# Performance work log

Measured on AMD Instinct MI355X. Metric: run time of the kernel, lower is better.

The kernel has to match this reference:

```python
import jax, jax.numpy as jnp
import numpy as np

DIM = 512
DIM2 = 2 * DIM
HEADS = 8
HEAD_DIM = DIM2 // HEADS
NB = 4                      # BlockDiagonalLinear blocks
BLK = DIM2 // NB
KS = 4                      # causal conv kernel size
EPS = 1e-5


def setup_inputs() -> dict:
    key = jax.random.key(0)
    ks = jax.random.split(key, 32)
    r = lambda i, shape, s=0.02: jax.random.normal(ks[i], shape, dtype=jnp.float32) * s
    inp = {
        "x": jax.random.normal(ks[0], (2, 2048, DIM), dtype=jnp.float32),
        "ln_w": jnp.ones((DIM,), jnp.float32),
        "ln_b": jnp.zeros((DIM,), jnp.float32),
        "mlp1_w": r(1, (DIM, DIM2)), "mlp1_b": jnp.zeros((DIM2,), jnp.float32),
        "mlp2_w": r(2, (DIM, DIM2)), "mlp2_b": jnp.zeros((DIM2,), jnp.float32),
        "conv_w": r(3, (DIM2, DIM2, KS)), "conv_b": jnp.zeros((DIM2,), jnp.float32),
        "bq_w": r(4, (NB, BLK, BLK)), "bk_w": r(5, (NB, BLK, BLK)), "bv_w": r(6, (NB, BLK, BLK)),
        "wq_w": r(7, (DIM2, DIM2)), "wq_b": jnp.zeros((DIM2,), jnp.float32),
        "wk_w": r(8, (DIM2, DIM2)), "wk_b": jnp.zeros((DIM2,), jnp.float32),
        "wv_w": r(9, (DIM2, DIM2)), "wv_b": jnp.zeros((DIM2,), jnp.float32),
        "wi_w": r(10, (DIM2, HEADS)), "wi_b": jnp.zeros((HEADS,), jnp.float32),
        "wf_w": r(11, (DIM2, HEADS)), "wf_b": jnp.zeros((HEADS,), jnp.float32),
        "gn_w": jnp.ones((DIM2,), jnp.float32), "gn_b": jnp.zeros((DIM2,), jnp.float32),
        "skip": jnp.ones((DIM2,), jnp.float32),
        "fin_w": r(12, (DIM2, DIM)), "fin_b": jnp.zeros((DIM,), jnp.float32),
    }
    return inp


def _layernorm(x, w, b):
    mu = jnp.mean(x, -1, keepdims=True)
    var = jnp.var(x, -1, keepdims=True)
    return (x - mu) * jax.lax.rsqrt(var + EPS) * w + b


def _block_linear(x, w):  # x: [b,s,DIM2], w: [NB, BLK, BLK]
    b, s, _ = x.shape
    xg = x.reshape(b, s, NB, BLK)
    return jnp.einsum('bsgi,gio->bsgo', xg, w).reshape(b, s, DIM2)


def _mlstm_cell(q, k, v, wq_w, wq_b, wk_w, wk_b, wv_w, wv_b,
                wi_w, wi_b, wf_w, wf_b, gn_w, gn_b):
    b, s, _ = q.shape
    tau = DIM2 ** 0.5
    itilde = jnp.einsum('bsd,dh->bhs', q, wi_w) + wi_b[None, :, None]   # [b,h,s]
    ftilde = jnp.einsum('bsd,dh->bhs', k, wf_w) + wf_b[None, :, None]   # [b,h,s]
    # cumulative log forget gates; F_act[i,j] = cs[i] - cs[j] on lower triangle
    cs = jnp.cumsum(jax.nn.log_sigmoid(ftilde), axis=-1)                # [b,h,s]
    mask = jnp.tril(jnp.ones((s, s), bool))
    Dtilde = jnp.where(mask,
                       cs[..., :, None] - cs[..., None, :] + itilde[..., None, :],
                       -jnp.inf)                                        # [b,h,s,s]
    max_d = jnp.max(Dtilde, axis=-1, keepdims=True)
    D = jnp.exp(Dtilde - max_d)
    qh = (q @ wq_w + wq_b).reshape(b, s, HEADS, HEAD_DIM).transpose(0, 2, 1, 3)
    kh = (k @ wk_w + wk_b).reshape(b, s, HEADS, HEAD_DIM).transpose(0, 2, 1, 3)
    vh = (v @ wv_w + wv_b).reshape(b, s, HEADS, HEAD_DIM).transpose(0, 2, 1, 3)
    Ctilde = jnp.einsum('bhid,bhjd->bhij', qh, kh) * D / tau
    maxit = jnp.maximum(jnp.abs(Ctilde.sum(-1)), jnp.exp(-max_d[..., 0]))  # [b,h,s]
    H = jnp.einsum('bhij,bhjd->bhid', Ctilde, vh) / (maxit[..., None] + 1e-8)
    H = H.transpose(0, 2, 1, 3)                                          # [b,s,h,hd]
    # GroupNorm(heads, DIM2): per (b,s,head-group) normalization
    mu = jnp.mean(H, -1, keepdims=True)
    var = jnp.var(H, -1, keepdims=True)
    Hn = (H - mu) * jax.lax.rsqrt(var + EPS)
    Hn = Hn * gn_w.reshape(HEADS, HEAD_DIM) + gn_b.reshape(HEADS, HEAD_DIM)
    return Hn.reshape(b, s, DIM2)


def reference(x, ln_w, ln_b, mlp1_w, mlp1_b, mlp2_w, mlp2_b, conv_w, conv_b,
              bq_w, bk_w, bv_w, wq_w, wq_b, wk_w, wk_b, wv_w, wv_b,
              wi_w, wi_b, wf_w, wf_b, gn_w, gn_b, skip, fin_w, fin_b):
    inputs = _layernorm(x, ln_w, ln_b)
    a = inputs @ mlp1_w + mlp1_b                 # [b,s,DIM2]
    bgate = jax.nn.silu(inputs @ mlp2_w + mlp2_b)
    # causal conv1d (left pad KS-1)
    ac = a.transpose(0, 2, 1)                    # [b,DIM2,s]
    qk = jax.lax.conv_general_dilated(ac, conv_w, (1,), [(KS - 1, 0)],
                                      dimension_numbers=('NCH', 'OIH', 'NCH'))
    qk = (qk + conv_b[None, :, None]).transpose(0, 2, 1)
    qk = jax.nn.silu(qk)
    q = _block_linear(qk, bq_w)
    k = _block_linear(qk, bk_w)
    v = _block_linear(a, bv_w)
    out1 = _mlstm_cell(q, k, v, wq_w, wq_b, wk_w, wk_b, wv_w, wv_b,
                       wi_w, wi_b, wf_w, wf_b, gn_w, gn_b)
    out1 = out1 + skip * qk
    out1 = out1 * bgate
    out1 = out1 @ fin_w + fin_b
    return x + out1
```

## Files before the change

### kernel.cpp

```cpp
#include <hip/hip_runtime.h>
#include <hip/hip_bf16.h>
#include <cmath>

typedef __hip_bfloat16 bf16;
typedef __attribute__((ext_vector_type(8))) short short8;
typedef __attribute__((ext_vector_type(4))) float f32x4;

#define SEQ   2048
#define DIMX  512
#define DIM2X 1024
#define NHEADS 8
#define HDIM  128
#define EPSF  1e-5f
#define PADROWS 2051

__device__ __forceinline__ float b2f(bf16 v) { return __bfloat162float(v); }
__device__ __forceinline__ bf16 f2b(float f) { return __float2bfloat16(f); }
__device__ __forceinline__ unsigned short f2bu(float f) { bf16 t = __float2bfloat16(f); return *(unsigned short*)&t; }

__device__ __forceinline__ void gl16(const bf16* g, bf16* l) {
  __builtin_amdgcn_global_load_lds((const __attribute__((address_space(1))) void*)g,
                                   (__attribute__((address_space(3))) void*)l, 16, 0, 0);
}

__global__ void __launch_bounds__(256) k_layernorm(const float* __restrict__ x,
                                                   const float* __restrict__ w,
                                                   const float* __restrict__ b,
                                                   bf16* __restrict__ out) {
  int row  = blockIdx.x * 4 + (threadIdx.x >> 6);
  int lane = threadIdx.x & 63;
  const float* xr = x + (size_t)row * DIMX;
  float v[8]; float s = 0.f, sq = 0.f;
#pragma unroll
  for (int i = 0; i < 8; i++) {
    float f = xr[lane + i * 64];
    v[i] = f; s += f; sq += f * f;
  }
#pragma unroll
  for (int off = 32; off; off >>= 1) { s += __shfl_xor(s, off); sq += __shfl_xor(sq, off); }
  float mu  = s * (1.f / DIMX);
  float var = sq * (1.f / DIMX) - mu * mu;
  float rs  = rsqrtf(var + EPSF);
  bf16* o = out + (size_t)row * DIMX;
#pragma unroll
  for (int i = 0; i < 8; i++) {
    int c = lane + i * 64;
    o[c] = f2b((v[i] - mu) * rs * w[c] + b[c]);
  }
}

__global__ void __launch_bounds__(256) k_castT3(const float* __restrict__ W0,
                                                const float* __restrict__ W1,
                                                const float* __restrict__ W2,
                                                bf16* __restrict__ WT,
                                                int K, int N, int innerZ, int gW, int gT) {
  __shared__ float t[32][33];
  const int z = blockIdx.z;
  const int sel = z / innerZ, zz = z % innerZ;
  const float* W = (sel == 0 ? W0 : sel == 1 ? W1 : W2) + (size_t)zz * gW;
  bf16* T = WT + (size_t)(sel * innerZ + zz) * gT;
  const int k0 = blockIdx.y * 32, n0 = blockIdx.x * 32;
  const int r = threadIdx.x >> 5, c = threadIdx.x & 31;
#pragma unroll
  for (int i = 0; i < 4; i++)
    t[r + i * 8][c] = W[(size_t)(k0 + r + i * 8) * N + n0 + c];
  __syncthreads();
#pragma unroll
  for (int i = 0; i < 4; i++)
    T[(size_t)(n0 + r + i * 8) * K + k0 + c] = f2b(t[c][r + i * 8]);
}

__global__ void __launch_bounds__(256) k_convwT(const float* __restrict__ cw, bf16* __restrict__ wc) {
  int idx = blockIdx.x * 256 + threadIdx.x;
  int o = idx >> 12, z = idx & 4095, kk = z >> 10, i = z & 1023;
  wc[idx] = f2b(cw[(size_t)o * 4096 + i * 4 + kk]);
}

__global__ void __launch_bounds__(256) k_zeropad(bf16* __restrict__ p) {
  int idx = blockIdx.x * 256 + threadIdx.x;
  int b = idx / 3072, off = idx % 3072;
  p[(size_t)b * PADROWS * DIM2X + off] = f2b(0.f);
}

__device__ __forceinline__ void mgemm_body(const bf16* A, int lda, const bf16* WT,
                                           const float* bias, void* Cv, const float* xres,
                                           int ldc, int K, int ACT, int STORE, int APAD,
                                           size_t coff) {
  __shared__ __align__(16) bf16 smA[128 * 32];
  __shared__ __align__(16) bf16 smB[64 * 32];
  const int tid  = threadIdx.x;
  const int lane = tid & 63;
  const int w = tid >> 6, wy = w >> 1, wx = w & 1;
  const int col = lane & 15, quad = lane >> 4;
  const int bm = blockIdx.y * 128, bn = blockIdx.x * 64;

  const int r4 = tid >> 2, c8 = (tid & 3) * 8;
  int ra0 = bm + r4, ra1 = bm + 64 + r4;
  if (APAD) { ra0 += (ra0 >> 11) * 3 + 3; ra1 += (ra1 >> 11) * 3 + 3; }
  const bf16* gA0 = A + (size_t)ra0 * lda + c8;
  const bf16* gA1 = A + (size_t)ra1 * lda + c8;
  const bf16* gB0 = WT + (size_t)(bn + r4) * K + c8;
  bf16* lA = &smA[r4 * 32 + c8];
  bf16* lB = &smB[r4 * 32 + c8];

  f32x4 acc[4][2];
#pragma unroll
  for (int a = 0; a < 4; a++)
#pragma unroll
    for (int b = 0; b < 2; b++) acc[a][b] = (f32x4){0.f, 0.f, 0.f, 0.f};

  const int laoff = (wy * 64) * 32, lboff = (wx * 32) * 32;
  for (int k0 = 0; k0 < K; k0 += 32) {
    gl16(gA0 + k0, lA);
    gl16(gA1 + k0, lA + 64 * 32);
    gl16(gB0 + k0, lB);
    asm volatile("s_waitcnt vmcnt(0)" ::: "memory");
    __syncthreads();
    short8 af[4], bfr[2];
#pragma unroll
    for (int mt = 0; mt < 4; mt++)
      af[mt] = *(const short8*)&smA[laoff + (mt * 16 + col) * 32 + quad * 8];
#pragma unroll
    for (int nt = 0; nt < 2; nt++)
      bfr[nt] = *(const short8*)&smB[lboff + (nt * 16 + col) * 32 + quad * 8];
#pragma unroll
    for (int mt = 0; mt < 4; mt++)
#pragma unroll
      for (int nt = 0; nt < 2; nt++)
        acc[mt][nt] = __builtin_amdgcn_mfma_f32_16x16x32_bf16(af[mt], bfr[nt], acc[mt][nt], 0, 0, 0);
    __syncthreads();
  }

#pragma unroll
  for (int mt = 0; mt < 4; mt++) {
#pragma unroll
    for (int nt = 0; nt < 2; nt++) {
      const int n = bn + wx * 32 + nt * 16 + col;
      const int mrow0 = bm + wy * 64 + mt * 16 + quad * 4;
      float bs = bias ? bias[n] : 0.f;
      if (STORE == 1) {
        bf16* C = (bf16*)Cv + coff;
        ushort4 pk;
        pk.x = f2bu(acc[mt][nt][0] + bs); pk.y = f2bu(acc[mt][nt][1] + bs);
        pk.z = f2bu(acc[mt][nt][2] + bs); pk.w = f2bu(acc[mt][nt][3] + bs);
        *(ushort4*)(C + (size_t)n * 4096 + mrow0) = pk;
      } else if (STORE == 2) {
        float* O = (float*)Cv + coff;
#pragma unroll
        for (int r = 0; r < 4; r++) {
          size_t gi = (size_t)(mrow0 + r) * ldc + n;
          O[gi] = acc[mt][nt][r] + bs + xres[gi];
        }
      } else if (STORE == 3) {
        bf16* C = (bf16*)Cv;
        const int pr = (mrow0 >> 11) * 3 + 3;
#pragma unroll
        for (int r = 0; r < 4; r++)
          C[(size_t)(mrow0 + pr + r) * ldc + n] = f2b(acc[mt][nt][r] + bs);
      } else {
        bf16* C = (bf16*)Cv + coff;
#pragma unroll
        for (int r = 0; r < 4; r++) {
          float v = acc[mt][nt][r] + bs;
          if (ACT == 1) v = v / (1.f + expf(-v));
          C[(size_t)(mrow0 + r) * ldc + n] = f2b(v);
        }
      }
    }
  }
}

template <int ACT, int STORE, int APAD>
__global__ void __launch_bounds__(256) k_mgemm(const bf16* __restrict__ A, int lda,
                                               const bf16* __restrict__ WT,
                                               const float* __restrict__ bias,
                                               void* __restrict__ Cv,
                                               const float* __restrict__ xres,
                                               int ldc, int K,
                                               int gA, int gW, int gC) {
  const int g = blockIdx.z;
  mgemm_body(A + (size_t)g * gA, lda, WT + (size_t)g * gW, bias, Cv, xres,
             ldc, K, ACT, STORE, APAD, (size_t)g * gC);
}

__global__ void __launch_bounds__(256) k_mgemmB(const bf16* A0, const bf16* A1, const bf16* A2,
                                                const bf16* W0, const bf16* W1, const bf16* W2,
                                                const float* b0, const float* b1, const float* b2,
                                                void* C0, void* C1, void* C2,
                                                int lda, int ldc, int K, int zPer,
                                                int gA, int gW, int gC,
                                                int actm, int storem, int apadm) {
  const int z = blockIdx.z;
  const int sel = z / zPer, zz = z % zPer;
  const bf16* A = (sel == 0 ? A0 : sel == 1 ? A1 : A2) + (size_t)zz * gA;
  const bf16* W = (sel == 0 ? W0 : sel == 1 ? W1 : W2) + (size_t)zz * gW;
  const float* bias = sel == 0 ? b0 : sel == 1 ? b1 : b2;
  void* Cv = sel == 0 ? C0 : sel == 1 ? C1 : C2;
  mgemm_body(A, lda, W, bias, Cv, nullptr, ldc, K,
             (actm >> sel) & 1, (storem >> (4 * sel)) & 15, (apadm >> sel) & 1,
             (size_t)zz * gC);
}

__global__ void __launch_bounds__(256) k_gates(const bf16* __restrict__ q, const bf16* __restrict__ kk,
                                               const float* __restrict__ wi, const float* __restrict__ wib,
                                               const float* __restrict__ wf, const float* __restrict__ wfb,
                                               float* __restrict__ it, float* __restrict__ ft) {
  int gid  = blockIdx.x * 4 + (threadIdx.x >> 6);
  int lane = threadIdx.x & 63;
  int which = gid >> 12;
  int m = gid & 4095;
  const bf16* row = (which ? kk : q) + (size_t)m * DIM2X;
  const float* w = which ? wf : wi;
  float s[8] = {0, 0, 0, 0, 0, 0, 0, 0};
  for (int d = lane; d < DIM2X; d += 64) {
    float xv = b2f(row[d]);
    const float4* wp = (const float4*)(w + d * 8);
    float4 w0 = wp[0], w1 = wp[1];
    s[0] += xv * w0.x; s[1] += xv * w0.y; s[2] += xv * w0.z; s[3] += xv * w0.w;
    s[4] += xv * w1.x; s[5] += xv * w1.y; s[6] += xv * w1.z; s[7] += xv * w1.w;
  }
#pragma unroll
  for (int off = 32; off; off >>= 1) {
#pragma unroll
    for (int h = 0; h < 8; h++) s[h] += __shfl_xor(s[h], off);
  }
  if (lane == 0) {
    int b_ = m >> 11, tt = m & 2047;
    const float* wb = which ? wfb : wib;
    float* dst = which ? ft : it;
#pragma unroll
    for (int h = 0; h < 8; h++)
      dst[((size_t)(b_ * NHEADS + h)) * SEQ + tt] = s[h] + wb[h];
  }
}

__global__ void __launch_bounds__(256) k_scan(const float* __restrict__ it, const float* __restrict__ ft,
                                              float* __restrict__ cs, float* __restrict__ md) {
  const int bh = blockIdx.x;
  const int t  = threadIdx.x;
  const float* fr = ft + (size_t)bh * SEQ;
  const float* ir = it + (size_t)bh * SEQ;
  float* csr = cs + (size_t)bh * SEQ;
  float* mdr = md + (size_t)bh * SEQ;
  __shared__ float tmp[256];
  float loc[8]; float run = 0.f;
#pragma unroll
  for (int j = 0; j < 8; j++) {
    float xv = fr[t * 8 + j];
    float ls = fminf(xv, 0.f) - log1pf(expf(-fabsf(xv)));
    run += ls; loc[j] = run;
  }
  tmp[t] = run;
  __syncthreads();
  for (int off = 1; off < 256; off <<= 1) {
    float add = (t >= off) ? tmp[t - off] : 0.f;
    __syncthreads();
    tmp[t] += add;
    __syncthreads();
  }
  float exc = (t == 0) ? 0.f : tmp[t - 1];
  float csv[8];
#pragma unroll
  for (int j = 0; j < 8; j++) { csv[j] = loc[j] + exc; csr[t * 8 + j] = csv[j]; }
  __syncthreads();
  float rmax = -INFINITY; float gm[8];
#pragma unroll
  for (int j = 0; j < 8; j++) {
    float gv = ir[t * 8 + j] - csv[j];
    rmax = fmaxf(rmax, gv); gm[j] = rmax;
  }
  tmp[t] = rmax;
  __syncthreads();
  for (int off = 1; off < 256; off <<= 1) {
    float other = (t >= off) ? tmp[t - off] : -INFINITY;
    __syncthreads();
    tmp[t] = fmaxf(tmp[t], other);
    __syncthreads();
  }
  float emax = (t == 0) ? -INFINITY : tmp[t - 1];
#pragma unroll
  for (int j = 0; j < 8; j++) mdr[t * 8 + j] = csv[j] + fmaxf(gm[j], emax);
}

__global__ void __launch_bounds__(256) k_attn_mfma(const bf16* __restrict__ qh,
                                                   const bf16* __restrict__ kh,
                                                   const bf16* __restrict__ vt,
                                                   const float* __restrict__ cs,
                                                   const float* __restrict__ md,
                                                   const float* __restrict__ itl,
                                                   bf16* __restrict__ Hout) {
  const int bh = blockIdx.y, b_ = bh >> 3, h = bh & 7;
  const int tile = 31 - blockIdx.x;
  const int i0 = tile * 64;
  const int tid = threadIdx.x;
  const int w = tid >> 6;
  const int lane = tid & 63;
  const int col = lane & 15, quad = lane >> 4;
  const int i0w = i0 + w * 16;
  const int iwmax = i0w + 15;
  const float L2E = 1.44269504f;

  __shared__ __align__(16) bf16 smK[2 * 4096];
  __shared__ __align__(16) bf16 smV[2 * 4096];
  __shared__ __align__(16) bf16 Sc[4][16][40];

  const size_t baseQK = ((size_t)b_ * SEQ) * DIM2X + (size_t)h * HDIM;
  const size_t vtb = (size_t)(h * HDIM) * 4096 + (size_t)b_ * SEQ;
  const float* csp = cs + (size_t)bh * SEQ;
  const float* mdp = md + (size_t)bh * SEQ;
  const float* itp = itl + (size_t)bh * SEQ;

  short8 qf[4];
#pragma unroll
  for (int kc = 0; kc < 4; kc++)
    qf[kc] = *(const short8*)(qh + baseQK + (size_t)(i0w + col) * DIM2X + kc * 32 + quad * 8);

  float cs_i[4], md_i[4];
#pragma unroll
  for (int r = 0; r < 4; r++) {
    int i = i0w + quad * 4 + r;
    cs_i[r] = csp[i] * L2E; md_i[r] = mdp[i] * L2E;
  }

  f32x4 accpv[8];
#pragma unroll
  for (int nb = 0; nb < 8; nb++) accpv[nb] = (f32x4){0.f, 0.f, 0.f, 0.f};
  float rs[4] = {0.f, 0.f, 0.f, 0.f};

  const int kj = tid >> 4, kq = tid & 15;
  const bf16* gKs = kh + baseQK + (size_t)kj * DIM2X + ((kq ^ (kj & 7)) * 8);
  const int vn = tid >> 2, vq = tid & 3;
  const bf16* gVs = vt + vtb + (size_t)vn * 4096 + ((vq ^ ((vn >> 1) & 3)) * 8);

  const int trips = 2 * tile + 2;

#define STAGE(buf, j0s)                                                        \
  do {                                                                         \
    bf16* dK = &smK[(buf) * 4096 + tid * 8];                                   \
    gl16(gKs + (size_t)(j0s) * DIM2X, dK);                                     \
    gl16(gKs + (size_t)((j0s) + 16) * DIM2X, dK + 2048);                       \
    bf16* dV = &smV[(buf) * 4096 + tid * 8];                                   \
    gl16(gVs + (j0s), dV);                                                     \
    gl16(gVs + (j0s) + (size_t)64 * 4096, dV + 2048);                          \
  } while (0)

  STAGE(0, 0);
  asm volatile("s_waitcnt vmcnt(0)" ::: "memory");
  __syncthreads();

  for (int t = 0; t < trips; ++t) {
    const int cur = t & 1;
    const int j0p = t * 32;
    if (t + 1 < trips) STAGE(cur ^ 1, j0p + 32);
    if (j0p <= iwmax) {
      float g0 = (itp[j0p + col] - csp[j0p + col]) * L2E;
      float g1 = (itp[j0p + 16 + col] - csp[j0p + 16 + col]) * L2E;
      const bool jt1 = (j0p + 16 <= iwmax);
#pragma unroll
      for (int jt = 0; jt < 2; jt++) {
        const int j0 = j0p + jt * 16;
        float sv[4] = {0.f, 0.f, 0.f, 0.f};
        if (jt == 0 || jt1) {
          const int jj = jt * 16 + col;
          f32x4 aq = (f32x4){0.f, 0.f, 0.f, 0.f};
#pragma unroll
          for (int kc = 0; kc < 4; kc++) {
            short8 bk = *(const short8*)&smK[cur * 4096 + jj * 128 + ((((kc << 2) | quad) ^ (jj & 7)) << 3)];
            aq = __builtin_amdgcn_mfma_f32_16x16x32_bf16(qf[kc], bk, aq, 0, 0, 0);
          }
          const int j = j0 + col;
          const float gj = jt ? g1 : g0;
#pragma unroll
          for (int r = 0; r < 4; r++) {
            const int i = i0w + quad * 4 + r;
            float s = (j <= i) ? exp2f(cs_i[r] + gj - md_i[r] - 5.f) * aq[r] : 0.f;
            sv[r] = s; rs[r] += s;
          }
        }
#pragma unroll
        for (int r = 0; r < 4; r++) Sc[w][quad * 4 + r][jt * 16 + col] = f2b(sv[r]);
      }
      asm volatile("s_waitcnt lgkmcnt(0)" ::: "memory");
      __builtin_amdgcn_sched_barrier(0);
      short8 af = *(const short8*)(&Sc[w][col][quad * 8]);
#pragma unroll
      for (int nb = 0; nb < 8; nb++) {
        const int rn = nb * 16 + col;
        short8 bv = *(const short8*)&smV[cur * 4096 + rn * 32 + ((quad ^ ((rn >> 1) & 3)) << 3)];
        accpv[nb] = __builtin_amdgcn_mfma_f32_16x16x32_bf16(af, bv, accpv[nb], 0, 0, 0);
      }
    }
    asm volatile("s_waitcnt vmcnt(0)" ::: "memory");
    __syncthreads();
  }
#undef STAGE

#pragma unroll
  for (int r = 0; r < 4; r++) {
    float v = rs[r];
    v += __shfl_xor(v, 1); v += __shfl_xor(v, 2);
    v += __shfl_xor(v, 4); v += __shfl_xor(v, 8);
    rs[r] = v;
  }
  float inv[4];
#pragma unroll
  for (int r = 0; r < 4; r++) {
    float maxit = fmaxf(fabsf(rs[r]), exp2f(fminf(-md_i[r], 43.f)));
    inv[r] = 1.f / (maxit + 1e-8f);
  }
#pragma unroll
  for (int nb = 0; nb < 8; nb++)
#pragma unroll
    for (int r = 0; r < 4; r++)
      Hout[baseQK + (size_t)(i0w + quad * 4 + r) * DIM2X + nb * 16 + col] = f2b(accpv[nb][r] * inv[r]);
}

__global__ void __launch_bounds__(256) k_gnorm(const bf16* __restrict__ H, const bf16* __restrict__ qk,
                                               const bf16* __restrict__ bg,
                                               const float* __restrict__ gw, const float* __restrict__ gb,
                                               const float* __restrict__ skip, bf16* __restrict__ pre) {
  int gid  = blockIdx.x * 4 + (threadIdx.x >> 6);
  int lane = threadIdx.x & 63;
  int m = gid >> 3, h = gid & 7;
  const bf16* Hr = H + (size_t)m * DIM2X + (size_t)h * HDIM;
  float v0 = b2f(Hr[lane]), v1 = b2f(Hr[lane + 64]);
  float s = v0 + v1, sq = v0 * v0 + v1 * v1;
#pragma unroll
  for (int off = 32; off; off >>= 1) { s += __shfl_xor(s, off); sq += __shfl_xor(sq, off); }
  float mu  = s * (1.f / 128.f);
  float var = sq * (1.f / 128.f) - mu * mu;
  float rs  = rsqrtf(var + EPSF);
#pragma unroll
  for (int e = 0; e < 2; e++) {
    int c = lane + e * 64;
    int col = h * HDIM + c;
    float v = e ? v1 : v0;
    float hn = (v - mu) * rs * gw[col] + gb[col];
    size_t gidx = (size_t)m * DIM2X + col;
    pre[gidx] = f2b((hn + skip[col] * b2f(qk[gidx])) * b2f(bg[gidx]));
  }
}

extern "C" void kernel_launch(void* const* d_in, const int* in_sizes, int n_in,
                              void* d_out, int out_size, void* d_ws, size_t ws_size,
                              hipStream_t stream) {
  const float* x     = (const float*)d_in[0];
  const float* ln_w  = (const float*)d_in[1];
  const float* ln_b  = (const float*)d_in[2];
  const float* mlp1w = (const float*)d_in[3];
  const float* mlp1b = (const float*)d_in[4];
  const float* mlp2w = (const float*)d_in[5];
  const float* mlp2b = (const float*)d_in[6];
  const float* convw = (const float*)d_in[7];
  const float* convb = (const float*)d_in[8];
  const float* bqw   = (const float*)d_in[9];
  const float* bkw   = (const float*)d_in[10];
  const float* bvw   = (const float*)d_in[11];
  const float* wqw   = (const float*)d_in[12];
  const float* wqb   = (const float*)d_in[13];
  const float* wkw   = (const float*)d_in[14];
  const float* wkb   = (const float*)d_in[15];
  const float* wvw   = (const float*)d_in[16];
  const float* wvb   = (const float*)d_in[17];
  const float* wiw   = (const float*)d_in[18];
  const float* wib   = (const float*)d_in[19];
  const float* wfw   = (const float*)d_in[20];
  const float* wfb   = (const float*)d_in[21];
  const float* gnw   = (const float*)d_in[22];
  const float* gnb   = (const float*)d_in[23];
  const float* skip  = (const float*)d_in[24];
  const float* finw  = (const float*)d_in[25];
  const float* finb  = (const float*)d_in[26];
  float* out = (float*)d_out;

  float* GA  = (float*)d_ws;
  float* ITb = GA;
  float* FTb = GA + 32768;
  float* CSb = GA + 65536;
  float* MDb = GA + 98304;
  const size_t SLOT = 4u * 1024u * 1024u;
  bf16* S0 = (bf16*)((char*)d_ws + (1 << 20));
  bf16* S1 = S0 + SLOT;
  bf16* S2 = S1 + SLOT;
  bf16* S3 = S2 + SLOT;
  bf16* S4 = S3 + SLOT;
  bf16* S5 = S4 + SLOT;
  bf16* S6 = S5 + SLOT;
  bf16 *LN = S0, *BG = S2, *QKb = S3, *Qb = S4, *Kb = S5, *Vb = S6;
  bf16 *QH = S0, *KH = S1, *VT = S4, *Hb = S5, *PRE = S6;
  bf16* WTb   = S6 + SLOT;
  bf16* mlp1T = WTb;
  bf16* mlp2T = WTb + 524288;
  bf16* convT = WTb + 1048576;
  bf16* bqT   = WTb + 5242880;
  bf16* bkT   = bqT + 262144;
  bf16* bvT   = bkT + 262144;
  bf16* wqT   = bvT + 262144;
  bf16* wkT   = wqT + 1048576;
  bf16* wvT   = wkT + 1048576;
  bf16* finT  = wvT + 1048576;
  bf16* APD   = finT + 524288;

  k_castT3<<<dim3(32, 16, 2), 256, 0, stream>>>(mlp1w, mlp2w, mlp2w, mlp1T, DIMX, DIM2X, 1, 0, 524288);
  k_castT3<<<dim3(32, 32, 3), 256, 0, stream>>>(wqw, wkw, wvw, wqT, DIM2X, DIM2X, 1, 0, 1048576);
  k_castT3<<<dim3(8, 8, 12), 256, 0, stream>>>(bqw, bkw, bvw, bqT, 256, 256, 4, 65536, 65536);
  k_castT3<<<dim3(16, 32, 1), 256, 0, stream>>>(finw, finw, finw, finT, DIM2X, DIMX, 1, 0, 524288);
  k_convwT<<<16384, 256, 0, stream>>>(convw, convT);
  k_zeropad<<<24, 256, 0, stream>>>(APD);

  k_layernorm<<<1024, 256, 0, stream>>>(x, ln_w, ln_b, LN);
  k_mgemmB<<<dim3(16, 32, 2), 256, 0, stream>>>(LN, LN, LN, mlp1T, mlp2T, mlp2T,
                                                mlp1b, mlp2b, mlp2b, APD, BG, BG,
                                                DIMX, DIM2X, DIMX, 1, 0, 0, 0,
                                                 0b10,  3 | (0 << 4),  0);
  k_mgemm<1, 0, 0><<<dim3(16, 16, 2), 256, 0, stream>>>(APD, DIM2X, convT, convb, QKb, nullptr,
                                                        DIM2X, 4096, PADROWS * DIM2X, 0, SEQ * DIM2X);
  k_mgemmB<<<dim3(4, 32, 12), 256, 0, stream>>>(QKb, QKb, APD, bqT, bkT, bvT,
                                                nullptr, nullptr, nullptr, Qb, Kb, Vb,
                                                DIM2X, DIM2X, 256, 4, 256, 65536, 256,
                                                 0,  0,  0b100);
  k_gates<<<2048, 256, 0, stream>>>(Qb, Kb, wiw, wib, wfw, wfb, ITb, FTb);
  k_scan<<<16, 256, 0, stream>>>(ITb, FTb, CSb, MDb);
  k_mgemmB<<<dim3(16, 32, 3), 256, 0, stream>>>(Qb, Kb, Vb, wqT, wkT, wvT,
                                                wqb, wkb, wvb, QH, KH, VT,
                                                DIM2X, DIM2X, DIM2X, 1, 0, 0, 0,
                                                 0,  0 | (0 << 4) | (1 << 8),  0);
  k_attn_mfma<<<dim3(32, 16), 256, 0, stream>>>(QH, KH, VT, CSb, MDb, ITb, Hb);
  k_gnorm<<<8192, 256, 0, stream>>>(Hb, QKb, BG, gnw, gnb, skip, PRE);
  k_mgemm<0, 2, 0><<<dim3(8, 32), 256, 0, stream>>>(PRE, DIM2X, finT, finb, out, x, DIMX, DIM2X, 0, 0, 0);
}
```

Baseline: 475.8 us.

## Deepen GEMM and attention LDS pipelines to four buffers with prefetch distance two

The GEMM body moves from a single LDS buffer with a full wait and two barriers per k-step to a 4-slot ring. Loads run two steps ahead, guarded by partial vmcnt waits and one barrier per step. The attention kernel gets the same treatment: its 2-slot K/V ring becomes 4 slots with prefetch distance two, and the tile order is reversed for odd batches to balance causal work across blocks. The cost is four times the LDS for these buffers, which can lower occupancy, and correctness now depends on the vmcnt counts and the single barrier being enough to avoid overwriting slots still being read.

```diff
diff --git a/kernel.cpp b/kernel.cpp
--- a/kernel.cpp
+++ b/kernel.cpp
@@ -86,8 +86,8 @@
                                            const float* bias, void* Cv, const float* xres,
                                            int ldc, int K, int ACT, int STORE, int APAD,
                                            size_t coff) {
-  __shared__ __align__(16) bf16 smA[128 * 32];
-  __shared__ __align__(16) bf16 smB[64 * 32];
+  __shared__ __align__(16) bf16 smA[4][128 * 32];
+  __shared__ __align__(16) bf16 smB[4][64 * 32];
   const int tid  = threadIdx.x;
   const int lane = tid & 63;
   const int w = tid >> 6, wy = w >> 1, wx = w & 1;
@@ -100,8 +100,6 @@
   const bf16* gA0 = A + (size_t)ra0 * lda + c8;
   const bf16* gA1 = A + (size_t)ra1 * lda + c8;
   const bf16* gB0 = WT + (size_t)(bn + r4) * K + c8;
-  bf16* lA = &smA[r4 * 32 + c8];
-  bf16* lB = &smB[r4 * 32 + c8];
 
   f32x4 acc[4][2];
 #pragma unroll
@@ -110,26 +108,41 @@
     for (int b = 0; b < 2; b++) acc[a][b] = (f32x4){0.f, 0.f, 0.f, 0.f};
 
   const int laoff = (wy * 64) * 32, lboff = (wx * 32) * 32;
-  for (int k0 = 0; k0 < K; k0 += 32) {
-    gl16(gA0 + k0, lA);
-    gl16(gA1 + k0, lA + 64 * 32);
-    gl16(gB0 + k0, lB);
-    asm volatile("s_waitcnt vmcnt(0)" ::: "memory");
-    __syncthreads();
+  const int lsa = r4 * 32 + c8;
+  const int nsteps = K >> 5;
+
+#define GSTAGE(buf, k0s)                                                       \
+  do {                                                                         \
+    gl16(gA0 + (k0s), &smA[buf][lsa]);                                         \
+    gl16(gA1 + (k0s), &smA[buf][64 * 32 + lsa]);                               \
+    gl16(gB0 + (k0s), &smB[buf][lsa]);                                         \
+  } while (0)
+
+  GSTAGE(0, 0);
+  if (nsteps > 1) GSTAGE(1, 32);
+  for (int s = 0; s < nsteps; ++s) {
+    if (s + 2 < nsteps) GSTAGE((s + 2) & 3, (s + 2) * 32);
+    if (s + 2 < nsteps)      asm volatile("s_waitcnt vmcnt(6)" ::: "memory");
+    else if (s + 1 < nsteps) asm volatile("s_waitcnt vmcnt(3)" ::: "memory");
+    else                     asm volatile("s_waitcnt vmcnt(0)" ::: "memory");
+    __builtin_amdgcn_s_barrier();
+    asm volatile("" ::: "memory");
+    const bf16* bA = smA[s & 3];
+    const bf16* bB = smB[s & 3];
     short8 af[4], bfr[2];
 #pragma unroll
     for (int mt = 0; mt < 4; mt++)
-      af[mt] = *(const short8*)&smA[laoff + (mt * 16 + col) * 32 + quad * 8];
+      af[mt] = *(const short8*)&bA[laoff + (mt * 16 + col) * 32 + quad * 8];
 #pragma unroll
     for (int nt = 0; nt < 2; nt++)
-      bfr[nt] = *(const short8*)&smB[lboff + (nt * 16 + col) * 32 + quad * 8];
+      bfr[nt] = *(const short8*)&bB[lboff + (nt * 16 + col) * 32 + quad * 8];
 #pragma unroll
     for (int mt = 0; mt < 4; mt++)
 #pragma unroll
       for (int nt = 0; nt < 2; nt++)
         acc[mt][nt] = __builtin_amdgcn_mfma_f32_16x16x32_bf16(af[mt], bfr[nt], acc[mt][nt], 0, 0, 0);
-    __syncthreads();
-  }
+  }
+#undef GSTAGE
 
 #pragma unroll
   for (int mt = 0; mt < 4; mt++) {
@@ -290,7 +303,8 @@
                                                    const float* __restrict__ itl,
                                                    bf16* __restrict__ Hout) {
   const int bh = blockIdx.y, b_ = bh >> 3, h = bh & 7;
-  const int tile = 31 - blockIdx.x;
+  const int bx = blockIdx.x;
+  const int tile = ((blockIdx.y >> 3) & 1) ? bx : 31 - bx;
   const int i0 = tile * 64;
   const int tid = threadIdx.x;
   const int w = tid >> 6;
@@ -300,8 +314,8 @@
   const int iwmax = i0w + 15;
   const float L2E = 1.44269504f;
 
-  __shared__ __align__(16) bf16 smK[2 * 4096];
-  __shared__ __align__(16) bf16 smV[2 * 4096];
+  __shared__ __align__(16) bf16 smK[4 * 4096];
+  __shared__ __align__(16) bf16 smV[4 * 4096];
   __shared__ __align__(16) bf16 Sc[4][16][40];
 
   const size_t baseQK = ((size_t)b_ * SEQ) * DIM2X + (size_t)h * HDIM;
@@ -345,13 +359,16 @@
   } while (0)
 
   STAGE(0, 0);
-  asm volatile("s_waitcnt vmcnt(0)" ::: "memory");
-  __syncthreads();
-
+  STAGE(1, 32);
   for (int t = 0; t < trips; ++t) {
-    const int cur = t & 1;
+    const int cur = t & 3;
     const int j0p = t * 32;
-    if (t + 1 < trips) STAGE(cur ^ 1, j0p + 32);
+    if (t + 2 < trips) STAGE((t + 2) & 3, j0p + 64);
+    if (t + 2 < trips)      asm volatile("s_waitcnt vmcnt(8)" ::: "memory");
+    else if (t + 1 < trips) asm volatile("s_waitcnt vmcnt(4)" ::: "memory");
+    else                    asm volatile("s_waitcnt vmcnt(0)" ::: "memory");
+    __builtin_amdgcn_s_barrier();
+    asm volatile("" ::: "memory");
     if (j0p <= iwmax) {
       float g0 = (itp[j0p + col] - csp[j0p + col]) * L2E;
       float g1 = (itp[j0p + 16 + col] - csp[j0p + 16 + col]) * L2E;
@@ -390,8 +407,6 @@
         accpv[nb] = __builtin_amdgcn_mfma_f32_16x16x32_bf16(af, bv, accpv[nb], 0, 0, 0);
       }
     }
-    asm volatile("s_waitcnt vmcnt(0)" ::: "memory");
-    __syncthreads();
   }
 #undef STAGE
 
```

Measured after the change: 471.7 us. No clear change (-0.9%).
